# Optimization experiments

Measured on AMD Instinct MI355X. Metric: run time of the kernel, lower is better.

Reference implementation:

```python
import jax, jax.numpy as jnp
import numpy as np

N = 100_000   # num nodes
E = 1_600_000 # num directed edges (avg degree 16)
F_IN = 128    # num_features
HID = 128     # hidden_channels
C = 64        # num_classes
BN_EPS = 1e-5


def setup_inputs() -> dict:
    key = jax.random.key(0)
    ks = jax.random.split(key, 12)
    x = jax.random.normal(ks[0], (N, F_IN), dtype=jnp.float32)
    edge_index = jax.random.randint(ks[1], (2, E), 0, N, dtype=jnp.int32)
    def lin(k, fi, fo):
        s = 1.0 / np.sqrt(fi)
        return jax.random.uniform(k, (fi, fo), jnp.float32, -s, s)
    W1 = lin(ks[2], F_IN, HID)
    b1 = jnp.zeros((HID,), jnp.float32)
    W2 = lin(ks[3], HID, HID)
    b2 = jnp.zeros((HID,), jnp.float32)
    Wout = lin(ks[4], F_IN + 2 * HID, C)  # skip concat: 128 + 2*128 = 384
    bout = jnp.zeros((C,), jnp.float32)
    gamma = jnp.ones((HID,), jnp.float32)   # shared BatchNorm1d weight
    beta = jnp.zeros((HID,), jnp.float32)
    return {"x": x, "edge_index": edge_index, "W1": W1, "b1": b1,
            "W2": W2, "b2": b2, "Wout": Wout, "bout": bout,
            "gamma": gamma, "beta": beta}


def _gcn_norm(edge_index, n):
    # add self loops, then symmetric normalization (PyG GCNConv default)
    src, dst = edge_index[0], edge_index[1]
    loop = jnp.arange(n, dtype=src.dtype)
    src = jnp.concatenate([src, loop])
    dst = jnp.concatenate([dst, loop])
    deg = jax.ops.segment_sum(jnp.ones(src.shape[0], jnp.float32), dst, num_segments=n)
    dinv = jnp.where(deg > 0, jax.lax.rsqrt(deg), 0.0)
    norm = dinv[src] * dinv[dst]  # [E+N]
    return src, dst, norm


def _gcn_conv(h, src, dst, norm, n, W, b):
    h = h @ W                         # [n, out]
    msg = h[src] * norm[:, None]      # gather + scale, [E+n, out]
    return jax.ops.segment_sum(msg, dst, num_segments=n) + b


def _batchnorm(h, gamma, beta):
    # BatchNorm1d in training mode: biased batch statistics over nodes
    m = jnp.mean(h, axis=0)
    v = jnp.mean((h - m) ** 2, axis=0)
    return gamma * (h - m) * jax.lax.rsqrt(v + BN_EPS) + beta


def reference(x, edge_index, W1, b1, W2, b2, Wout, bout, gamma, beta):
    n = x.shape[0]
    src, dst, norm = _gcn_norm(edge_index, n)
    h1 = _batchnorm(jax.nn.relu(_gcn_conv(x, src, dst, norm, n, W1, b1)), gamma, beta)
    h2 = _batchnorm(jax.nn.relu(_gcn_conv(h1, src, dst, norm, n, W2, b2)), gamma, beta)
    hcat = jnp.concatenate([x, h1, h2], axis=1)  # skip concat [n, 384]
    return jax.nn.relu(_gcn_conv(hcat, src, dst, norm, n, Wout, bout))
```

## Files before the change

kernel.cpp:

```cpp
#include <hip/hip_runtime.h>
#include <cstdint>
#include <cstddef>

#define BN_EPS 1e-5f
#define NBLK 256
#define EPBMAX 6400
#define BCAP 4096
#define NBANK 32

typedef __attribute__((ext_vector_type(8))) short  bf16x8;
typedef __attribute__((ext_vector_type(4))) float  f32x4;
typedef __attribute__((ext_vector_type(8))) unsigned short ushort8;

__device__ __forceinline__ float bf2f(unsigned short u) {
  union { unsigned int i; float f; } c; c.i = ((unsigned int)u) << 16; return c.f;
}
__device__ __forceinline__ unsigned short f2bf(float f) {
  union { float f; unsigned int i; } c; c.f = f;
  unsigned int u = c.i;
  return (unsigned short)((u + 0x7FFFu + ((u >> 16) & 1u)) >> 16);
}

__global__ __launch_bounds__(256) void k_part(const int* __restrict__ src, const int* __restrict__ dst, int e, int epb,
                                              int* __restrict__ pairsG, int* __restrict__ cntT, int* __restrict__ scanT,
                                              int* __restrict__ totals,
                                              const float* __restrict__ W1, const float* __restrict__ W2,
                                              const float* __restrict__ W3,
                                              unsigned short* __restrict__ Wt1, unsigned short* __restrict__ Wt2,
                                              unsigned short* __restrict__ Wt3) {
  int b = blockIdx.x, tid = threadIdx.x;
  if (b >= NBLK) {
    int bb = b - NBLK;
    if (bb < 64)       { int idx = bb * 256 + tid;        Wt1[(idx & 127) * 128 + (idx >> 7)] = f2bf(W1[idx]); }
    else if (bb < 128) { int idx = (bb - 64) * 256 + tid; Wt2[(idx & 127) * 128 + (idx >> 7)] = f2bf(W2[idx]); }
    else               { int idx = (bb - 128) * 256 + tid; Wt3[(idx & 63) * 384 + (idx >> 6)] = f2bf(W3[idx]); }
    return;
  }
  __shared__ int sbuf[EPBMAX];
  __shared__ int hist[1024];
  __shared__ int base[1024];
  __shared__ int tmp[256];
  int e0 = b * epb, e1 = min(e0 + epb, e);
  for (int i = tid; i < 1024; i += 256) hist[i] = 0;
  __syncthreads();
  for (int i = e0 + tid; i < e1; i += 256) atomicAdd(&hist[dst[i] >> 7], 1);
  __syncthreads();
  for (int i = tid; i < 1024; i += 256) { int h = hist[i]; if (h) atomicAdd(&totals[i], h); }
  int c0 = hist[tid * 4], c1 = hist[tid * 4 + 1], c2 = hist[tid * 4 + 2], c3 = hist[tid * 4 + 3];
  int lsum = c0 + c1 + c2 + c3;
  tmp[tid] = lsum; __syncthreads();
  for (int off = 1; off < 256; off <<= 1) {
    int t = (tid >= off) ? tmp[tid - off] : 0; __syncthreads();
    tmp[tid] += t; __syncthreads();
  }
  int excl = tmp[tid] - lsum;
  base[tid * 4] = excl; base[tid * 4 + 1] = excl + c0;
  base[tid * 4 + 2] = excl + c0 + c1; base[tid * 4 + 3] = excl + c0 + c1 + c2;
  *(int4*)(cntT + b * 1024 + tid * 4) = make_int4(c0, c1, c2, c3);
  *(int4*)(scanT + b * 1024 + tid * 4) = make_int4(base[tid * 4], base[tid * 4 + 1], base[tid * 4 + 2], base[tid * 4 + 3]);
  __syncthreads();
  for (int i = e0 + tid; i < e1; i += 256) {
    int d = dst[i], s = src[i];
    int p = atomicAdd(&base[d >> 7], 1);
    sbuf[p] = ((d & 127) << 25) | s;
  }
  __syncthreads();
  int cnt = e1 - e0;
  for (int i = tid; i < cnt; i += 256) pairsG[e0 + i] = sbuf[i];
}

__global__ __launch_bounds__(1024) void k_bscan(const int* __restrict__ totals, int* __restrict__ bbase, int nb, int e) {
  __shared__ int tmp[1024];
  int tid = threadIdx.x;
  int v = (tid < nb) ? totals[tid] : 0;
  tmp[tid] = v; __syncthreads();
  for (int off = 1; off < 1024; off <<= 1) {
    int t = (tid >= off) ? tmp[tid - off] : 0; __syncthreads();
    tmp[tid] += t; __syncthreads();
  }
  if (tid < nb) bbase[tid] = tmp[tid] - v;
  if (tid == 0) bbase[nb] = e;
}

__global__ __launch_bounds__(256) void k_build(const int* __restrict__ pairsG, const int* __restrict__ cntT,
                                               const int* __restrict__ scanT, const int* __restrict__ bbase_,
                                               int epb, int n, int nb,
                                               int* __restrict__ rowptr, int* __restrict__ colG, float* __restrict__ dinvG) {
  __shared__ int lpair[BCAP];
  __shared__ int lcol[BCAP];
  __shared__ int lcnt[128], lcur[128];
  __shared__ int tmp[256];
  int k = blockIdx.x, tid = threadIdx.x;
  int len = cntT[tid * 1024 + k];
  int sbase = tid * epb + scanT[tid * 1024 + k];
  tmp[tid] = len; __syncthreads();
  for (int off = 1; off < 256; off <<= 1) {
    int t = (tid >= off) ? tmp[tid - off] : 0; __syncthreads();
    tmp[tid] += t; __syncthreads();
  }
  int dpos = tmp[tid] - len;
  int cnt = tmp[255];
  for (int i = 0; i < len; ++i) lpair[dpos + i] = pairsG[sbase + i];
  if (tid < 128) lcnt[tid] = 0;
  __syncthreads();
  for (int j = tid; j < cnt; j += 256) atomicAdd(&lcnt[((unsigned)lpair[j]) >> 25], 1);
  __syncthreads();
  if (tid < 128) tmp[tid] = lcnt[tid];
  __syncthreads();
  for (int off = 1; off < 128; off <<= 1) {
    int t = (tid >= off && tid < 128) ? tmp[tid - off] : 0; __syncthreads();
    if (tid < 128) tmp[tid] += t;
    __syncthreads();
  }
  int bb = bbase_[k];
  if (tid < 128) {
    int excl = tmp[tid] - lcnt[tid];
    lcur[tid] = excl;
    int g = k * 128 + tid;
    if (g < n) {
      rowptr[g] = bb + excl;
      dinvG[g] = rsqrtf((float)lcnt[tid] + 1.0f);
    }
  }
  if (k == nb - 1 && tid == 0) rowptr[n] = bb + cnt;
  __syncthreads();
  for (int j = tid; j < cnt; j += 256) {
    int w = lpair[j];
    int p = atomicAdd(&lcur[((unsigned)w) >> 25], 1);
    lcol[p] = w & 0x01FFFFFF;
  }
  __syncthreads();
  for (int j = tid; j < cnt; j += 256) colG[bb + j] = lcol[j];
}

template <int MODE>
__global__ __launch_bounds__(256) void k_gemm128(const void* __restrict__ Ap, const unsigned short* __restrict__ Bt,
                                                 const float* __restrict__ bank, const float* __restrict__ gamma,
                                                 const float* __restrict__ beta, float invN,
                                                 const float* __restrict__ dinv, unsigned short* __restrict__ C, int n) {
  __shared__ unsigned short Bs[128 * 128];
  __shared__ float ssl[256];
  const int tid = threadIdx.x;
  const int row0 = blockIdx.x * 128;
  if (MODE == 1 && tid < 128) {
    float s = 0.f, q = 0.f;
    for (int b = 0; b < NBANK; ++b) { s += bank[b * 256 + tid]; q += bank[b * 256 + 128 + tid]; }
    float m = s * invN, var = q * invN - m * m;
    float sc = gamma[tid] * rsqrtf(var + BN_EPS);
    ssl[tid] = sc; ssl[128 + tid] = beta[tid] - m * sc;
  }
  {
    int colr = tid >> 1;
    int cbase = (tid & 1) * 8;
#pragma unroll
    for (int i = 0; i < 8; ++i) {
      int c16 = (cbase + i) * 16;
      int dstb = colr * 256 + (c16 ^ ((colr & 7) << 4));
      ushort8 v = *reinterpret_cast<const ushort8*>(Bt + colr * 128 + (c16 >> 1));
      *reinterpret_cast<ushort8*>((char*)Bs + dstb) = v;
    }
  }
  __syncthreads();

  const int wv = tid >> 6, l = tid & 63, lr = l & 15, lk = l >> 4;
  int rowc[2];
#pragma unroll
  for (int mi = 0; mi < 2; ++mi) {
    int gr = row0 + wv * 32 + mi * 16 + lr;
    rowc[mi] = (gr < n) ? gr : 0;
  }

  bf16x8 aF[2][4];
  if (MODE == 0) {
    const float* A = (const float*)Ap;
#pragma unroll
    for (int mi = 0; mi < 2; ++mi)
#pragma unroll
      for (int kt = 0; kt < 4; ++kt) {
        const float* p = A + (size_t)rowc[mi] * 128 + kt * 32 + lk * 8;
        f32x4 lo = *reinterpret_cast<const f32x4*>(p);
        f32x4 hi = *reinterpret_cast<const f32x4*>(p + 4);
        bf16x8 a;
#pragma unroll
        for (int j = 0; j < 4; ++j) { a[j] = (short)f2bf(lo[j]); a[4 + j] = (short)f2bf(hi[j]); }
        aF[mi][kt] = a;
      }
  } else {
    const unsigned short* A = (const unsigned short*)Ap;
    ushort8 raw[2][4];
#pragma unroll
    for (int mi = 0; mi < 2; ++mi)
#pragma unroll
      for (int kt = 0; kt < 4; ++kt)
        raw[mi][kt] = *reinterpret_cast<const ushort8*>(A + (size_t)rowc[mi] * 128 + kt * 32 + lk * 8);
#pragma unroll
    for (int kt = 0; kt < 4; ++kt) {
      int kof = kt * 32 + lk * 8;
      float sc[8], sh[8];
#pragma unroll
      for (int j = 0; j < 8; ++j) { sc[j] = ssl[kof + j]; sh[j] = ssl[128 + kof + j]; }
#pragma unroll
      for (int mi = 0; mi < 2; ++mi) {
        bf16x8 a;
#pragma unroll
        for (int j = 0; j < 8; ++j) a[j] = (short)f2bf(bf2f(raw[mi][kt][j]) * sc[j] + sh[j]);
        aF[mi][kt] = a;
      }
    }
  }

  f32x4 acc[2][8];
#pragma unroll
  for (int mi = 0; mi < 2; ++mi)
#pragma unroll
    for (int ni = 0; ni < 8; ++ni) acc[mi][ni] = (f32x4)0.f;

#pragma unroll
  for (int kt = 0; kt < 4; ++kt) {
    int kbyte = kt * 64 + lk * 16;
    bf16x8 bF[8];
#pragma unroll
    for (int ni = 0; ni < 8; ++ni) {
      int c = ni * 16 + lr;
      bF[ni] = *reinterpret_cast<bf16x8*>((char*)Bs + c * 256 + (kbyte ^ ((c & 7) << 4)));
    }
#pragma unroll
    for (int mi = 0; mi < 2; ++mi)
#pragma unroll
      for (int ni = 0; ni < 8; ++ni)
        acc[mi][ni] = __builtin_amdgcn_mfma_f32_16x16x32_bf16(aF[mi][kt], bF[ni], acc[mi][ni], 0, 0, 0);
  }

#pragma unroll
  for (int mi = 0; mi < 2; ++mi) {
#pragma unroll
    for (int i = 0; i < 4; ++i) {
      int gr = row0 + wv * 32 + mi * 16 + lk * 4 + i;
      if (gr < n) {
        float di = dinv[gr];
#pragma unroll
        for (int ni = 0; ni < 8; ++ni) {
          int gc = ni * 16 + lr;
          C[(size_t)gr * 128 + gc] = f2bf(acc[mi][ni][i] * di);
        }
      }
    }
  }
}

__global__ __launch_bounds__(256) void k_gemm3(const float* __restrict__ x, const unsigned short* __restrict__ a1,
                                               const unsigned short* __restrict__ a2,
                                               const float* __restrict__ bank1, const float* __restrict__ bank2,
                                               const float* __restrict__ gamma, const float* __restrict__ beta,
                                               float invN,
                                               const unsigned short* __restrict__ Bt3, const float* __restrict__ dinv,
                                               unsigned short* __restrict__ C, int n) {
  __shared__ unsigned short Bs[64 * 384];
  __shared__ float ssl[512];
  const int tid = threadIdx.x;
  const int row0 = blockIdx.x * 128;
  if (tid < 256) {
    int f = tid & 127;
    const float* bk = (tid < 128) ? bank1 : bank2;
    int base = (tid < 128) ? 0 : 256;
    float s = 0.f, q = 0.f;
    for (int b = 0; b < NBANK; ++b) { s += bk[b * 256 + f]; q += bk[b * 256 + 128 + f]; }
    float m = s * invN, var = q * invN - m * m;
    float sc = gamma[f] * rsqrtf(var + BN_EPS);
    ssl[base + f] = sc; ssl[base + 128 + f] = beta[f] - m * sc;
  }
  {
    int colr = tid >> 2;
    int cb = tid & 3;
#pragma unroll
    for (int i = 0; i < 12; ++i) {
      int c16 = (cb + 4 * i) * 16;
      int dstb = colr * 768 + (c16 ^ ((colr & 7) << 4));
      ushort8 v = *reinterpret_cast<const ushort8*>(Bt3 + colr * 384 + (c16 >> 1));
      *reinterpret_cast<ushort8*>((char*)Bs + dstb) = v;
    }
  }
  __syncthreads();

  const int wv = tid >> 6, l = tid & 63, lr = l & 15, lk = l >> 4;
  int rowc[2];
#pragma unroll
  for (int mi = 0; mi < 2; ++mi) {
    int gr = row0 + wv * 32 + mi * 16 + lr;
    rowc[mi] = (gr < n) ? gr : 0;
  }

  f32x4 acc[2][4];
#pragma unroll
  for (int mi = 0; mi < 2; ++mi)
#pragma unroll
    for (int ni = 0; ni < 4; ++ni) acc[mi][ni] = (f32x4)0.f;

#pragma unroll
  for (int ch = 0; ch < 3; ++ch) {
    bf16x8 aF[2][4];
    if (ch == 0) {
#pragma unroll
      for (int mi = 0; mi < 2; ++mi)
#pragma unroll
        for (int kt = 0; kt < 4; ++kt) {
          const float* p = x + (size_t)rowc[mi] * 128 + kt * 32 + lk * 8;
          f32x4 lo = *reinterpret_cast<const f32x4*>(p);
          f32x4 hi = *reinterpret_cast<const f32x4*>(p + 4);
          bf16x8 a;
#pragma unroll
          for (int j = 0; j < 4; ++j) { a[j] = (short)f2bf(lo[j]); a[4 + j] = (short)f2bf(hi[j]); }
          aF[mi][kt] = a;
        }
    } else {
      const unsigned short* A = (ch == 1) ? a1 : a2;
      int base = (ch == 1) ? 0 : 256;
      ushort8 raw[2][4];
#pragma unroll
      for (int mi = 0; mi < 2; ++mi)
#pragma unroll
        for (int kt = 0; kt < 4; ++kt)
          raw[mi][kt] = *reinterpret_cast<const ushort8*>(A + (size_t)rowc[mi] * 128 + kt * 32 + lk * 8);
#pragma unroll
      for (int kt = 0; kt < 4; ++kt) {
        int kof = kt * 32 + lk * 8;
        float sc[8], sh[8];
#pragma unroll
        for (int j = 0; j < 8; ++j) { sc[j] = ssl[base + kof + j]; sh[j] = ssl[base + 128 + kof + j]; }
#pragma unroll
        for (int mi = 0; mi < 2; ++mi) {
          bf16x8 a;
#pragma unroll
          for (int j = 0; j < 8; ++j) a[j] = (short)f2bf(bf2f(raw[mi][kt][j]) * sc[j] + sh[j]);
          aF[mi][kt] = a;
        }
      }
    }
#pragma unroll
    for (int kt = 0; kt < 4; ++kt) {
      int kbyteB = ch * 256 + kt * 64 + lk * 16;
      bf16x8 bF[4];
#pragma unroll
      for (int ni = 0; ni < 4; ++ni) {
        int c = ni * 16 + lr;
        bF[ni] = *reinterpret_cast<bf16x8*>((char*)Bs + c * 768 + (kbyteB ^ ((c & 7) << 4)));
      }
#pragma unroll
      for (int mi = 0; mi < 2; ++mi)
#pragma unroll
        for (int ni = 0; ni < 4; ++ni)
          acc[mi][ni] = __builtin_amdgcn_mfma_f32_16x16x32_bf16(aF[mi][kt], bF[ni], acc[mi][ni], 0, 0, 0);
    }
  }

#pragma unroll
  for (int mi = 0; mi < 2; ++mi) {
#pragma unroll
    for (int i = 0; i < 4; ++i) {
      int gr = row0 + wv * 32 + mi * 16 + lk * 4 + i;
      if (gr < n) {
        float di = dinv[gr];
#pragma unroll
        for (int ni = 0; ni < 4; ++ni) {
          int gc = ni * 16 + lr;
          C[(size_t)gr * 64 + gc] = f2bf(acc[mi][ni][i] * di);
        }
      }
    }
  }
}

template <int F, int STATS, int OUT_F32>
__global__ __launch_bounds__(256) void k_agg(const unsigned short* __restrict__ t, const int* __restrict__ rowptr,
                                             const int* __restrict__ col, const float* __restrict__ dinv,
                                             const float* __restrict__ bias, void* __restrict__ outp,
                                             float* __restrict__ bank, int n) {
  const int G = F / 8;
  const int RPB = 256 / G;
  int g = threadIdx.x / G;
  int c = threadIdx.x % G;
  int r = blockIdx.x * RPB + g;
  bool act = (r < n);
  float v[8];
#pragma unroll
  for (int j = 0; j < 8; ++j) v[j] = 0.f;
  int f0 = c * 8;
  if (act) {
    float di = dinv[r];
    int e = rowptr[r];
    int e1 = rowptr[r + 1];
    float acc[8];
    {
      ushort8 sv = *reinterpret_cast<const ushort8*>(t + (size_t)r * F + f0);
#pragma unroll
      for (int j = 0; j < 8; ++j) acc[j] = bf2f(sv[j]);
    }
    for (; e + 8 <= e1; e += 8) {
      int s0 = col[e],     s1 = col[e + 1], s2 = col[e + 2], s3 = col[e + 3];
      int s4 = col[e + 4], s5 = col[e + 5], s6 = col[e + 6], s7 = col[e + 7];
      ushort8 u0 = *reinterpret_cast<const ushort8*>(t + (size_t)s0 * F + f0);
      ushort8 u1 = *reinterpret_cast<const ushort8*>(t + (size_t)s1 * F + f0);
      ushort8 u2 = *reinterpret_cast<const ushort8*>(t + (size_t)s2 * F + f0);
      ushort8 u3 = *reinterpret_cast<const ushort8*>(t + (size_t)s3 * F + f0);
      ushort8 u4 = *reinterpret_cast<const ushort8*>(t + (size_t)s4 * F + f0);
      ushort8 u5 = *reinterpret_cast<const ushort8*>(t + (size_t)s5 * F + f0);
      ushort8 u6 = *reinterpret_cast<const ushort8*>(t + (size_t)s6 * F + f0);
      ushort8 u7 = *reinterpret_cast<const ushort8*>(t + (size_t)s7 * F + f0);
#pragma unroll
      for (int j = 0; j < 8; ++j) {
        float p0 = bf2f(u0[j]) + bf2f(u1[j]);
        float p1 = bf2f(u2[j]) + bf2f(u3[j]);
        float p2 = bf2f(u4[j]) + bf2f(u5[j]);
        float p3 = bf2f(u6[j]) + bf2f(u7[j]);
        acc[j] += (p0 + p1) + (p2 + p3);
      }
    }
    if (e + 4 <= e1) {
      int s0 = col[e], s1 = col[e + 1], s2 = col[e + 2], s3 = col[e + 3];
      ushort8 u0 = *reinterpret_cast<const ushort8*>(t + (size_t)s0 * F + f0);
      ushort8 u1 = *reinterpret_cast<const ushort8*>(t + (size_t)s1 * F + f0);
      ushort8 u2 = *reinterpret_cast<const ushort8*>(t + (size_t)s2 * F + f0);
      ushort8 u3 = *reinterpret_cast<const ushort8*>(t + (size_t)s3 * F + f0);
#pragma unroll
      for (int j = 0; j < 8; ++j)
        acc[j] += (bf2f(u0[j]) + bf2f(u1[j])) + (bf2f(u2[j]) + bf2f(u3[j]));
      e += 4;
    }
    if (e + 2 <= e1) {
      int s0 = col[e], s1 = col[e + 1];
      ushort8 u0 = *reinterpret_cast<const ushort8*>(t + (size_t)s0 * F + f0);
      ushort8 u1 = *reinterpret_cast<const ushort8*>(t + (size_t)s1 * F + f0);
#pragma unroll
      for (int j = 0; j < 8; ++j) acc[j] += bf2f(u0[j]) + bf2f(u1[j]);
      e += 2;
    }
    if (e < e1) {
      int s = col[e];
      ushort8 u = *reinterpret_cast<const ushort8*>(t + (size_t)s * F + f0);
#pragma unroll
      for (int j = 0; j < 8; ++j) acc[j] += bf2f(u[j]);
    }
#pragma unroll
    for (int j = 0; j < 8; ++j) v[j] = fmaxf(acc[j] * di + bias[f0 + j], 0.f);
    if (OUT_F32) {
      float* o = (float*)outp;
#pragma unroll
      for (int j = 0; j < 8; j += 4) {
        f32x4 w = {v[j], v[j + 1], v[j + 2], v[j + 3]};
        __builtin_nontemporal_store(w, reinterpret_cast<f32x4*>(o + (size_t)r * F + f0 + j));
      }
    } else {
      ushort8 ov;
#pragma unroll
      for (int j = 0; j < 8; ++j) ov[j] = f2bf(v[j]);
      *reinterpret_cast<ushort8*>((unsigned short*)outp + (size_t)r * F + f0) = ov;
    }
  }
  if (STATS) {
    __shared__ float sA[256 * 8];
    __shared__ float sB[256 * 8];
#pragma unroll
    for (int j = 0; j < 8; ++j) { sA[threadIdx.x * 8 + j] = v[j]; sB[threadIdx.x * 8 + j] = v[j] * v[j]; }
    __syncthreads();
    if (threadIdx.x < 128) {
      int f = threadIdx.x;
      int cc = f >> 3, jj = f & 7;
      float s = 0.f, q = 0.f;
#pragma unroll
      for (int gg = 0; gg < 16; ++gg) {
        s += sA[(gg * 16 + cc) * 8 + jj];
        q += sB[(gg * 16 + cc) * 8 + jj];
      }
      float* bk = bank + (blockIdx.x & (NBANK - 1)) * 256;
      atomicAdd(&bk[f], s);
      atomicAdd(&bk[128 + f], q);
    }
  }
}

extern "C" void kernel_launch(void* const* d_in, const int* in_sizes, int n_in,
                              void* d_out, int out_size, void* d_ws, size_t ws_size,
                              hipStream_t stream) {
  const float* x    = (const float*)d_in[0];
  const int*   ei   = (const int*)d_in[1];
  const float* W1   = (const float*)d_in[2];
  const float* b1   = (const float*)d_in[3];
  const float* W2   = (const float*)d_in[4];
  const float* b2   = (const float*)d_in[5];
  const float* Wout = (const float*)d_in[6];
  const float* bout = (const float*)d_in[7];
  const float* gamma= (const float*)d_in[8];
  const float* beta = (const float*)d_in[9];
  float* out = (float*)d_out;

  const int n = in_sizes[0] / 128;
  const int e = in_sizes[1] / 2;
  const int* src = ei;
  const int* dst = ei + e;
  const int nb = (n + 127) >> 7;
  const int epb = (e + NBLK - 1) / NBLK;

  char* ws = (char*)d_ws;
  size_t off = 0;
  auto alloc = [&](size_t bytes) -> void* {
    void* p = ws + off;
    off += (bytes + 255) & ~(size_t)255;
    return p;
  };
  int*   pairsG = (int*)alloc((size_t)NBLK * epb * 4);
  int*   cntT   = (int*)alloc((size_t)NBLK * 1024 * 4);
  int*   scanT  = (int*)alloc((size_t)NBLK * 1024 * 4);
  int*   totals = (int*)alloc(1024 * 4);
  float* bank1  = (float*)alloc(NBANK * 256 * 4);
  float* bank2  = (float*)alloc(NBANK * 256 * 4);
  int*   bbase  = (int*)alloc(1025 * 4);
  int*   rowptr = (int*)alloc(((size_t)n + 1) * 4);
  float* dinv   = (float*)alloc((size_t)n * 4);
  int*   col    = (int*)alloc((size_t)e * 4);
  unsigned short* Wt1 = (unsigned short*)alloc(128 * 128 * 2);
  unsigned short* Wt2 = (unsigned short*)alloc(128 * 128 * 2);
  unsigned short* Wt3 = (unsigned short*)alloc(384 * 64 * 2);
  unsigned short* t   = (unsigned short*)alloc((size_t)n * 128 * 2);
  unsigned short* a1  = (unsigned short*)alloc((size_t)n * 128 * 2);
  unsigned short* a2  = (unsigned short*)alloc((size_t)n * 128 * 2);

  hipMemsetAsync(totals, 0, 1024 * 4 + (size_t)2 * NBANK * 256 * 4, stream);

  k_part<<<NBLK + 224, 256, 0, stream>>>(src, dst, e, epb, pairsG, cntT, scanT, totals,
                                         W1, W2, Wout, Wt1, Wt2, Wt3);
  k_bscan<<<1, 1024, 0, stream>>>(totals, bbase, nb, e);
  k_build<<<nb, 256, 0, stream>>>(pairsG, cntT, scanT, bbase, epb, n, nb, rowptr, col, dinv);

  int nbG = (n + 127) / 128;
  int nbA128 = (n + 15) / 16;
  int nbA64 = (n + 31) / 32;
  float invN = 1.f / (float)n;

  k_gemm128<0><<<nbG, 256, 0, stream>>>(x, Wt1, nullptr, nullptr, nullptr, invN, dinv, t, n);
  k_agg<128, 1, 0><<<nbA128, 256, 0, stream>>>(t, rowptr, col, dinv, b1, a1, bank1, n);

  k_gemm128<1><<<nbG, 256, 0, stream>>>(a1, Wt2, bank1, gamma, beta, invN, dinv, t, n);
  k_agg<128, 1, 0><<<nbA128, 256, 0, stream>>>(t, rowptr, col, dinv, b2, a2, bank2, n);

  k_gemm3<<<nbG, 256, 0, stream>>>(x, a1, a2, bank1, bank2, gamma, beta, invN, Wt3, dinv, t, n);
  k_agg<64, 0, 1><<<nbA64, 256, 0, stream>>>(t, rowptr, col, dinv, bout, out, nullptr, n);
}
```

Measured before the change: 273.6 us.

## Store intermediate features in 16-column slabs and aggregate per slab; fold block scan into build

Result: slower. 460.0 us (+68.1%).

```diff
diff --git a/kernel.cpp b/kernel.cpp
--- a/kernel.cpp
+++ b/kernel.cpp
@@ -69,28 +69,28 @@
   for (int i = tid; i < cnt; i += 256) pairsG[e0 + i] = sbuf[i];
 }
 
-__global__ __launch_bounds__(1024) void k_bscan(const int* __restrict__ totals, int* __restrict__ bbase, int nb, int e) {
-  __shared__ int tmp[1024];
-  int tid = threadIdx.x;
-  int v = (tid < nb) ? totals[tid] : 0;
-  tmp[tid] = v; __syncthreads();
-  for (int off = 1; off < 1024; off <<= 1) {
-    int t = (tid >= off) ? tmp[tid - off] : 0; __syncthreads();
-    tmp[tid] += t; __syncthreads();
-  }
-  if (tid < nb) bbase[tid] = tmp[tid] - v;
-  if (tid == 0) bbase[nb] = e;
-}
-
 __global__ __launch_bounds__(256) void k_build(const int* __restrict__ pairsG, const int* __restrict__ cntT,
-                                               const int* __restrict__ scanT, const int* __restrict__ bbase_,
+                                               const int* __restrict__ scanT, const int* __restrict__ totals,
                                                int epb, int n, int nb,
                                                int* __restrict__ rowptr, int* __restrict__ colG, float* __restrict__ dinvG) {
   __shared__ int lpair[BCAP];
   __shared__ int lcol[BCAP];
   __shared__ int lcnt[128], lcur[128];
   __shared__ int tmp[256];
+  __shared__ int bbs;
   int k = blockIdx.x, tid = threadIdx.x;
+  {
+    int part = 0;
+    for (int i = tid; i < k; i += 256) part += totals[i];
+    tmp[tid] = part; __syncthreads();
+    for (int s = 128; s > 0; s >>= 1) {
+      if (tid < s) tmp[tid] += tmp[tid + s];
+      __syncthreads();
+    }
+    if (tid == 0) bbs = tmp[0];
+    __syncthreads();
+  }
+  int bb = bbs;
   int len = cntT[tid * 1024 + k];
   int sbase = tid * epb + scanT[tid * 1024 + k];
   tmp[tid] = len; __syncthreads();
@@ -112,7 +112,6 @@
     if (tid < 128) tmp[tid] += t;
     __syncthreads();
   }
-  int bb = bbase_[k];
   if (tid < 128) {
     int excl = tmp[tid] - lcnt[tid];
     lcur[tid] = excl;
@@ -191,8 +190,10 @@
 #pragma unroll
     for (int mi = 0; mi < 2; ++mi)
 #pragma unroll
-      for (int kt = 0; kt < 4; ++kt)
-        raw[mi][kt] = *reinterpret_cast<const ushort8*>(A + (size_t)rowc[mi] * 128 + kt * 32 + lk * 8);
+      for (int kt = 0; kt < 4; ++kt) {
+        int slab = kt * 2 + (lk >> 1);
+        raw[mi][kt] = *reinterpret_cast<const ushort8*>(A + (size_t)slab * n * 16 + (size_t)rowc[mi] * 16 + (lk & 1) * 8);
+      }
 #pragma unroll
     for (int kt = 0; kt < 4; ++kt) {
       int kof = kt * 32 + lk * 8;
@@ -239,10 +240,8 @@
       if (gr < n) {
         float di = dinv[gr];
 #pragma unroll
-        for (int ni = 0; ni < 8; ++ni) {
-          int gc = ni * 16 + lr;
-          C[(size_t)gr * 128 + gc] = f2bf(acc[mi][ni][i] * di);
-        }
+        for (int ni = 0; ni < 8; ++ni)
+          C[(size_t)ni * n * 16 + (size_t)gr * 16 + lr] = f2bf(acc[mi][ni][i] * di);
       }
     }
   }
@@ -319,8 +318,10 @@
 #pragma unroll
       for (int mi = 0; mi < 2; ++mi)
 #pragma unroll
-        for (int kt = 0; kt < 4; ++kt)
-          raw[mi][kt] = *reinterpret_cast<const ushort8*>(A + (size_t)rowc[mi] * 128 + kt * 32 + lk * 8);
+        for (int kt = 0; kt < 4; ++kt) {
+          int slab = kt * 2 + (lk >> 1);
+          raw[mi][kt] = *reinterpret_cast<const ushort8*>(A + (size_t)slab * n * 16 + (size_t)rowc[mi] * 16 + (lk & 1) * 8);
+        }
 #pragma unroll
       for (int kt = 0; kt < 4; ++kt) {
         int kof = kt * 32 + lk * 8;
@@ -361,51 +362,54 @@
       if (gr < n) {
         float di = dinv[gr];
 #pragma unroll
-        for (int ni = 0; ni < 4; ++ni) {
-          int gc = ni * 16 + lr;
-          C[(size_t)gr * 64 + gc] = f2bf(acc[mi][ni][i] * di);
-        }
-      }
-    }
-  }
-}
-
-template <int F, int STATS, int OUT_F32>
-__global__ __launch_bounds__(256) void k_agg(const unsigned short* __restrict__ t, const int* __restrict__ rowptr,
-                                             const int* __restrict__ col, const float* __restrict__ dinv,
-                                             const float* __restrict__ bias, void* __restrict__ outp,
-                                             float* __restrict__ bank, int n) {
-  const int G = F / 8;
-  const int RPB = 256 / G;
-  int g = threadIdx.x / G;
-  int c = threadIdx.x % G;
-  int r = blockIdx.x * RPB + g;
-  bool act = (r < n);
+        for (int ni = 0; ni < 4; ++ni)
+          C[(size_t)ni * n * 16 + (size_t)gr * 16 + lr] = f2bf(acc[mi][ni][i] * di);
+      }
+    }
+  }
+}
+
+template <int STATS>
+__global__ __launch_bounds__(256) void k_agg128s(const unsigned short* __restrict__ t, const int* __restrict__ rowptr,
+                                                 const int* __restrict__ col, const float* __restrict__ dinv,
+                                                 const float* __restrict__ bias, unsigned short* __restrict__ outp,
+                                                 float* __restrict__ bank, int n) {
+  int bid = blockIdx.x;
+  int slab = bid & 7, chunk = bid >> 3;
+  int tid = threadIdx.x;
+  int g = tid >> 1, h = tid & 1;
+  int r = chunk * 128 + g;
+  const unsigned short* ts = t + (size_t)slab * n * 16;
+  int hb = h * 8;
   float v[8];
 #pragma unroll
   for (int j = 0; j < 8; ++j) v[j] = 0.f;
-  int f0 = c * 8;
-  if (act) {
+  if (r < n) {
     float di = dinv[r];
-    int e = rowptr[r];
-    int e1 = rowptr[r + 1];
+    int e = rowptr[r], e1 = rowptr[r + 1];
     float acc[8];
     {
-      ushort8 sv = *reinterpret_cast<const ushort8*>(t + (size_t)r * F + f0);
+      ushort8 sv = *reinterpret_cast<const ushort8*>(ts + (size_t)r * 16 + hb);
 #pragma unroll
       for (int j = 0; j < 8; ++j) acc[j] = bf2f(sv[j]);
     }
     for (; e + 8 <= e1; e += 8) {
-      int s0 = col[e],     s1 = col[e + 1], s2 = col[e + 2], s3 = col[e + 3];
-      int s4 = col[e + 4], s5 = col[e + 5], s6 = col[e + 6], s7 = col[e + 7];
-      ushort8 u0 = *reinterpret_cast<const ushort8*>(t + (size_t)s0 * F + f0);
-      ushort8 u1 = *reinterpret_cast<const ushort8*>(t + (size_t)s1 * F + f0);
-      ushort8 u2 = *reinterpret_cast<const ushort8*>(t + (size_t)s2 * F + f0);
-      ushort8 u3 = *reinterpret_cast<const ushort8*>(t + (size_t)s3 * F + f0);
-      ushort8 u4 = *reinterpret_cast<const ushort8*>(t + (size_t)s4 * F + f0);
-      ushort8 u5 = *reinterpret_cast<const ushort8*>(t + (size_t)s5 * F + f0);
-      ushort8 u6 = *reinterpret_cast<const ushort8*>(t + (size_t)s6 * F + f0);
-      ushort8 u7 = *reinterpret_cast<const ushort8*>(t + (size_t)s7 * F + f0);
+      int s0 = __builtin_nontemporal_load(col + e);
+      int s1 = __builtin_nontemporal_load(col + e + 1);
+      int s2 = __builtin_nontemporal_load(col + e + 2);
+      int s3 = __builtin_nontemporal_load(col + e + 3);
+      int s4 = __builtin_nontemporal_load(col + e + 4);
+      int s5 = __builtin_nontemporal_load(col + e + 5);
+      int s6 = __builtin_nontemporal_load(col + e + 6);
+      int s7 = __builtin_nontemporal_load(col + e + 7);
+      ushort8 u0 = *reinterpret_cast<const ushort8*>(ts + (size_t)s0 * 16 + hb);
+      ushort8 u1 = *reinterpret_cast<const ushort8*>(ts + (size_t)s1 * 16 + hb);
+      ushort8 u2 = *reinterpret_cast<const ushort8*>(ts + (size_t)s2 * 16 + hb);
+      ushort8 u3 = *reinterpret_cast<const ushort8*>(ts + (size_t)s3 * 16 + hb);
+      ushort8 u4 = *reinterpret_cast<const ushort8*>(ts + (size_t)s4 * 16 + hb);
+      ushort8 u5 = *reinterpret_cast<const ushort8*>(ts + (size_t)s5 * 16 + hb);
+      ushort8 u6 = *reinterpret_cast<const ushort8*>(ts + (size_t)s6 * 16 + hb);
+      ushort8 u7 = *reinterpret_cast<const ushort8*>(ts + (size_t)s7 * 16 + hb);
 #pragma unroll
       for (int j = 0; j < 8; ++j) {
         float p0 = bf2f(u0[j]) + bf2f(u1[j]);
@@ -415,67 +419,108 @@
         acc[j] += (p0 + p1) + (p2 + p3);
       }
     }
-    if (e + 4 <= e1) {
-      int s0 = col[e], s1 = col[e + 1], s2 = col[e + 2], s3 = col[e + 3];
-      ushort8 u0 = *reinterpret_cast<const ushort8*>(t + (size_t)s0 * F + f0);
-      ushort8 u1 = *reinterpret_cast<const ushort8*>(t + (size_t)s1 * F + f0);
-      ushort8 u2 = *reinterpret_cast<const ushort8*>(t + (size_t)s2 * F + f0);
-      ushort8 u3 = *reinterpret_cast<const ushort8*>(t + (size_t)s3 * F + f0);
-#pragma unroll
-      for (int j = 0; j < 8; ++j)
-        acc[j] += (bf2f(u0[j]) + bf2f(u1[j])) + (bf2f(u2[j]) + bf2f(u3[j]));
-      e += 4;
-    }
-    if (e + 2 <= e1) {
-      int s0 = col[e], s1 = col[e + 1];
-      ushort8 u0 = *reinterpret_cast<const ushort8*>(t + (size_t)s0 * F + f0);
-      ushort8 u1 = *reinterpret_cast<const ushort8*>(t + (size_t)s1 * F + f0);
-#pragma unroll
-      for (int j = 0; j < 8; ++j) acc[j] += bf2f(u0[j]) + bf2f(u1[j]);
-      e += 2;
-    }
-    if (e < e1) {
-      int s = col[e];
-      ushort8 u = *reinterpret_cast<const ushort8*>(t + (size_t)s * F + f0);
+    for (; e < e1; ++e) {
+      int s = __builtin_nontemporal_load(col + e);
+      ushort8 u = *reinterpret_cast<const ushort8*>(ts + (size_t)s * 16 + hb);
 #pragma unroll
       for (int j = 0; j < 8; ++j) acc[j] += bf2f(u[j]);
     }
 #pragma unroll
-    for (int j = 0; j < 8; ++j) v[j] = fmaxf(acc[j] * di + bias[f0 + j], 0.f);
-    if (OUT_F32) {
-      float* o = (float*)outp;
-#pragma unroll
-      for (int j = 0; j < 8; j += 4) {
-        f32x4 w = {v[j], v[j + 1], v[j + 2], v[j + 3]};
-        __builtin_nontemporal_store(w, reinterpret_cast<f32x4*>(o + (size_t)r * F + f0 + j));
-      }
-    } else {
-      ushort8 ov;
-#pragma unroll
-      for (int j = 0; j < 8; ++j) ov[j] = f2bf(v[j]);
-      *reinterpret_cast<ushort8*>((unsigned short*)outp + (size_t)r * F + f0) = ov;
-    }
+    for (int j = 0; j < 8; ++j) v[j] = fmaxf(acc[j] * di + bias[slab * 16 + hb + j], 0.f);
+    ushort8 ov;
+#pragma unroll
+    for (int j = 0; j < 8; ++j) ov[j] = f2bf(v[j]);
+    *reinterpret_cast<ushort8*>(outp + (size_t)slab * n * 16 + (size_t)r * 16 + hb) = ov;
   }
   if (STATS) {
     __shared__ float sA[256 * 8];
     __shared__ float sB[256 * 8];
 #pragma unroll
-    for (int j = 0; j < 8; ++j) { sA[threadIdx.x * 8 + j] = v[j]; sB[threadIdx.x * 8 + j] = v[j] * v[j]; }
+    for (int j = 0; j < 8; ++j) { sA[tid * 8 + j] = v[j]; sB[tid * 8 + j] = v[j] * v[j]; }
     __syncthreads();
-    if (threadIdx.x < 128) {
-      int f = threadIdx.x;
-      int cc = f >> 3, jj = f & 7;
-      float s = 0.f, q = 0.f;
-#pragma unroll
-      for (int gg = 0; gg < 16; ++gg) {
-        s += sA[(gg * 16 + cc) * 8 + jj];
-        q += sB[(gg * 16 + cc) * 8 + jj];
-      }
-      float* bk = bank + (blockIdx.x & (NBANK - 1)) * 256;
-      atomicAdd(&bk[f], s);
-      atomicAdd(&bk[128 + f], q);
-    }
-  }
+    for (int s = 64; s > 0; s >>= 1) {
+      if (g < s) {
+#pragma unroll
+        for (int j = 0; j < 8; ++j) {
+          sA[tid * 8 + j] += sA[(tid + 2 * s) * 8 + j];
+          sB[tid * 8 + j] += sB[(tid + 2 * s) * 8 + j];
+        }
+      }
+      __syncthreads();
+    }
+    if (g == 0) {
+      float* bk = bank + (chunk & (NBANK - 1)) * 256;
+      int f = slab * 16 + hb;
+#pragma unroll
+      for (int j = 0; j < 8; ++j) {
+        atomicAdd(&bk[f + j], sA[tid * 8 + j]);
+        atomicAdd(&bk[128 + f + j], sB[tid * 8 + j]);
+      }
+    }
+  }
+}
+
+__global__ __launch_bounds__(256) void k_agg64s(const unsigned short* __restrict__ t, const int* __restrict__ rowptr,
+                                                const int* __restrict__ col, const float* __restrict__ dinv,
+                                                const float* __restrict__ bias, float* __restrict__ outp, int n) {
+  int bid = blockIdx.x;
+  int jj = bid & 7, chunk = bid >> 3;
+  int slab = jj >> 1, rh = jj & 1;
+  int tid = threadIdx.x;
+  int g = tid >> 1, h = tid & 1;
+  int r = chunk * 256 + rh * 128 + g;
+  const unsigned short* ts = t + (size_t)slab * n * 16;
+  int hb = h * 8;
+  if (r >= n) return;
+  float di = dinv[r];
+  int e = rowptr[r], e1 = rowptr[r + 1];
+  float acc[8];
+  {
+    ushort8 sv = *reinterpret_cast<const ushort8*>(ts + (size_t)r * 16 + hb);
+#pragma unroll
+    for (int j = 0; j < 8; ++j) acc[j] = bf2f(sv[j]);
+  }
+  for (; e + 8 <= e1; e += 8) {
+    int s0 = __builtin_nontemporal_load(col + e);
+    int s1 = __builtin_nontemporal_load(col + e + 1);
+    int s2 = __builtin_nontemporal_load(col + e + 2);
+    int s3 = __builtin_nontemporal_load(col + e + 3);
+    int s4 = __builtin_nontemporal_load(col + e + 4);
+    int s5 = __builtin_nontemporal_load(col + e + 5);
+    int s6 = __builtin_nontemporal_load(col + e + 6);
+    int s7 = __builtin_nontemporal_load(col + e + 7);
+    ushort8 u0 = *reinterpret_cast<const ushort8*>(ts + (size_t)s0 * 16 + hb);
+    ushort8 u1 = *reinterpret_cast<const ushort8*>(ts + (size_t)s1 * 16 + hb);
+    ushort8 u2 = *reinterpret_cast<const ushort8*>(ts + (size_t)s2 * 16 + hb);
+    ushort8 u3 = *reinterpret_cast<const ushort8*>(ts + (size_t)s3 * 16 + hb);
+    ushort8 u4 = *reinterpret_cast<const ushort8*>(ts + (size_t)s4 * 16 + hb);
+    ushort8 u5 = *reinterpret_cast<const ushort8*>(ts + (size_t)s5 * 16 + hb);
+    ushort8 u6 = *reinterpret_cast<const ushort8*>(ts + (size_t)s6 * 16 + hb);
+    ushort8 u7 = *reinterpret_cast<const ushort8*>(ts + (size_t)s7 * 16 + hb);
+#pragma unroll
+    for (int j = 0; j < 8; ++j) {
+      float p0 = bf2f(u0[j]) + bf2f(u1[j]);
+      float p1 = bf2f(u2[j]) + bf2f(u3[j]);
+      float p2 = bf2f(u4[j]) + bf2f(u5[j]);
+      float p3 = bf2f(u6[j]) + bf2f(u7[j]);
+      acc[j] += (p0 + p1) + (p2 + p3);
+    }
+  }
+  for (; e < e1; ++e) {
+    int s = __builtin_nontemporal_load(col + e);
+    ushort8 u = *reinterpret_cast<const ushort8*>(ts + (size_t)s * 16 + hb);
+#pragma unroll
+    for (int j = 0; j < 8; ++j) acc[j] += bf2f(u[j]);
+  }
+  int fg = slab * 16 + hb;
+  float v[8];
+#pragma unroll
+  for (int j = 0; j < 8; ++j) v[j] = fmaxf(acc[j] * di + bias[fg + j], 0.f);
+  float* o = outp + (size_t)r * 64 + fg;
+  f32x4 w0 = {v[0], v[1], v[2], v[3]};
+  f32x4 w1 = {v[4], v[5], v[6], v[7]};
+  __builtin_nontemporal_store(w0, reinterpret_cast<f32x4*>(o));
+  __builtin_nontemporal_store(w1, reinterpret_cast<f32x4*>(o + 4));
 }
 
 extern "C" void kernel_launch(void* const* d_in, const int* in_sizes, int n_in,
@@ -513,7 +558,6 @@
   int*   totals = (int*)alloc(1024 * 4);
   float* bank1  = (float*)alloc(NBANK * 256 * 4);
   float* bank2  = (float*)alloc(NBANK * 256 * 4);
-  int*   bbase  = (int*)alloc(1025 * 4);
   int*   rowptr = (int*)alloc(((size_t)n + 1) * 4);
   float* dinv   = (float*)alloc((size_t)n * 4);
   int*   col    = (int*)alloc((size_t)e * 4);
@@ -528,20 +572,19 @@
 
   k_part<<<NBLK + 224, 256, 0, stream>>>(src, dst, e, epb, pairsG, cntT, scanT, totals,
                                          W1, W2, Wout, Wt1, Wt2, Wt3);
-  k_bscan<<<1, 1024, 0, stream>>>(totals, bbase, nb, e);
-  k_build<<<nb, 256, 0, stream>>>(pairsG, cntT, scanT, bbase, epb, n, nb, rowptr, col, dinv);
+  k_build<<<nb, 256, 0, stream>>>(pairsG, cntT, scanT, totals, epb, n, nb, rowptr, col, dinv);
 
   int nbG = (n + 127) / 128;
-  int nbA128 = (n + 15) / 16;
-  int nbA64 = (n + 31) / 32;
+  int nbA128 = ((n + 127) / 128) * 8;
+  int nbA64 = ((n + 255) / 256) * 8;
   float invN = 1.f / (float)n;
 
   k_gemm128<0><<<nbG, 256, 0, stream>>>(x, Wt1, nullptr, nullptr, nullptr, invN, dinv, t, n);
-  k_agg<128, 1, 0><<<nbA128, 256, 0, stream>>>(t, rowptr, col, dinv, b1, a1, bank1, n);
+  k_agg128s<1><<<nbA128, 256, 0, stream>>>(t, rowptr, col, dinv, b1, a1, bank1, n);
 
   k_gemm128<1><<<nbG, 256, 0, stream>>>(a1, Wt2, bank1, gamma, beta, invN, dinv, t, n);
-  k_agg<128, 1, 0><<<nbA128, 256, 0, stream>>>(t, rowptr, col, dinv, b2, a2, bank2, n);
+  k_agg128s<1><<<nbA128, 256, 0, stream>>>(t, rowptr, col, dinv, b2, a2, bank2, n);
 
   k_gemm3<<<nbG, 256, 0, stream>>>(x, a1, a2, bank1, bank2, gamma, beta, invN, Wt3, dinv, t, n);
-  k_agg<64, 0, 1><<<nbA64, 256, 0, stream>>>(t, rowptr, col, dinv, bout, out, nullptr, n);
-}
+  k_agg64s<<<nbA64, 256, 0, stream>>>(t, rowptr, col, dinv, bout, out, n);
+}
```
